# Optimization experiments

Hardware: AMD Instinct MI355X
Metric: run time of the kernel (lower is better)

The kernel has to match this reference:

```python
import jax, jax.numpy as jnp
from jax import lax
import numpy as np

B, S = 128, 512
TARGET_SIZE = 32
T = TARGET_SIZE + 4  # tag_size, START = T-2, END = T-1


def setup_inputs() -> dict:
    key = jax.random.key(0)
    k1, k2, k3, k4 = jax.random.split(key, 4)
    feats = jax.random.normal(k1, (B, S, T), dtype=jnp.float32)
    # contiguous-prefix mask (lengths in [S//2, S])
    lengths = jax.random.randint(k2, (B,), S // 2, S + 1)
    mask = (jnp.arange(S)[None, :] < lengths[:, None]).astype(jnp.int32)
    tags = jax.random.randint(k3, (B, S), 0, TARGET_SIZE).astype(jnp.int32)
    # learned transitions, with the hard constraints from __init__
    transitions = 0.1 * jax.random.normal(k4, (T, T), dtype=jnp.float32)
    transitions = transitions.at[:, T - 2].set(-1000.0)  # nothing -> START
    transitions = transitions.at[T - 1, :].set(-1000.0)  # END -> nothing
    return {"feats": feats, "transitions": transitions, "mask": mask, "tags": tags}


def _nll(feats, transitions, mask, tags):
    # feats: (B,S,T), transitions: (T,T) with [i,j] = score(prev=i -> cur=j)
    b, s, t = feats.shape
    START, END = t - 2, t - 1
    fdtype = feats.dtype

    feats_t = jnp.swapaxes(feats, 0, 1)   # (S,B,T)
    mask_t = jnp.swapaxes(mask, 0, 1)     # (S,B)

    # ---- forward algorithm (partition function) ----
    # scores[t,b,i,j] = feats[b,t,j] + transitions[i,j]
    part0 = feats_t[0] + transitions[START][None, :]  # (B,T): alpha after step 0

    def step(part, xs):
        f_step, m_step = xs  # (B,T), (B,)
        # cur[b,i,j] = feats[b,j] + trans[i,j] + part[b,i]
        cur = f_step[:, None, :] + transitions[None, :, :] + part[:, :, None]
        new_part = jax.nn.logsumexp(cur, axis=1)  # (B,T)
        part = jnp.where(m_step[:, None].astype(bool), new_part, part)
        return part, None

    part, _ = lax.scan(step, part0, (feats_t[1:], mask_t[1:]))
    final = jax.nn.logsumexp(part[:, :, None] + transitions[None, :, :], axis=1)  # (B,T)
    forward_score = jnp.sum(final[:, END])

    # ---- gold score ----
    tags_i = tags.astype(jnp.int32)
    prev_tags = jnp.concatenate(
        [jnp.full((b, 1), START, dtype=jnp.int32), tags_i[:, :-1]], axis=1)  # (B,S)
    emit = jnp.take_along_axis(feats, tags_i[:, :, None], axis=2)[:, :, 0]    # (B,S)
    trans_sc = transitions[prev_tags, tags_i]                                  # (B,S)
    tg_energy = jnp.sum((emit + trans_sc) * mask.astype(fdtype))
    lengths = jnp.sum(mask, axis=1).astype(jnp.int32)                          # (B,)
    end_ids = jnp.take_along_axis(tags_i, (lengths - 1)[:, None], axis=1)[:, 0]
    end_energy = jnp.sum(transitions[end_ids, END])
    gold_score = tg_energy + end_energy

    # average_batch = True
    return (forward_score - gold_score) / jnp.asarray(b, fdtype)


def reference(feats, transitions, mask, tags):
    return _nll(feats, transitions, mask, tags)
```

## Files before the change

kernel.cpp:

```cpp
#include <hip/hip_runtime.h>
#include <hip/hip_bf16.h>


namespace {
constexpr int kB = 128;
constexpr int kS = 512;
constexpr int kT = 36;
constexpr int kStart = 34;
constexpr int kEnd = 35;
constexpr int kP = 16;
constexpr int kL = 32;
constexpr int kHStr = 72;
constexpr int kEStr = 64;

typedef __bf16 bf16x8 __attribute__((ext_vector_type(8)));
typedef __bf16 bf16x4 __attribute__((ext_vector_type(4)));
typedef float f32x4 __attribute__((ext_vector_type(4)));

__device__ __forceinline__ float readlane_f(float v, int lane) {
    return __builtin_bit_cast(float, __builtin_amdgcn_readlane(__builtin_bit_cast(int, v), lane));
}

__device__ __forceinline__ float wave_sum(float v) {
#pragma unroll
    for (int off = 32; off; off >>= 1) v += __shfl_xor(v, off, 64);
    return v;
}

__device__ __forceinline__ int wave_sum_i(int v) {
#pragma unroll
    for (int off = 32; off; off >>= 1) v += __shfl_xor(v, off, 64);
    return v;
}


__global__ __attribute__((amdgpu_flat_work_group_size(64, 64),
                          amdgpu_waves_per_eu(2, 4)))
void crf_chunk_kernel(const float* __restrict__ feats,
                      const float* __restrict__ trans,
                      const int* __restrict__ mask,
                      __bf16* __restrict__ Hws,
                      float* __restrict__ lscws) {
    const int b = blockIdx.x;
    const int p = blockIdx.y;
    const int tid = threadIdx.x;
    const int ln = tid & 15;
    const int quad = tid >> 4;

    __shared__ __align__(16) unsigned short Hlds[48 * kHStr];
    __shared__ __align__(16) float Etab[kL * kEStr];

    const int* mb = mask + b * kS;
    int len = 0;
    for (int k = tid; k < kS; k += 64) len += mb[k];
    len = wave_sum_i(len);

    __bf16* Hout = Hws + (size_t)(b * kP + p) * (kT * kT);
    const int cs = (p == 0) ? 1 : p * kL;
    const int ce = min((p + 1) * kL, len);
    const int nsteps = ce - cs;

    if (nsteps <= 0) {
        for (int idx = tid; idx < kT * kT; idx += 64)
            Hout[idx] = (__bf16)((idx / kT == idx % kT) ? 1.f : 0.f);
        if (tid == 0) lscws[b * kP + p] = 0.f;
        return;
    }

    for (int idx = tid; idx < 48 * kHStr; idx += 64) Hlds[idx] = 0;
    for (int r = tid; r < kT; r += 64) Hlds[r * kHStr + r] = 0x3F80;

    const float* fb = feats + ((size_t)b * kS + cs) * kT;
    for (int tl2 = 0; tl2 < kL; ++tl2)
        Etab[tl2 * kEStr + tid] = (tid < kT) ? __expf(fb[tl2 * kT + tid]) : 1.0f;

    auto afrag = [&](int rt, int kc) {
        bf16x8 r;
        const int j = rt * 16 + ln;
#pragma unroll
        for (int e = 0; e < 8; ++e) {
            const int k = kc * 32 + quad * 8 + e;
            float v = 0.f;
            if (k < kT && j < kT) v = __expf(trans[k * kT + j]);
            r[e] = (__bf16)v;
        }
        return r;
    };
    const bf16x8 a00 = afrag(0, 0), a01 = afrag(0, 1);
    const bf16x8 a10 = afrag(1, 0), a11 = afrag(1, 1);
    const bf16x8 a20 = afrag(2, 0), a21 = afrag(2, 1);

    float logC = 0.f;
    f32x4 c00, c01, c02, c10, c11, c12, c20, c21, c22;
    const f32x4 z = {0.f, 0.f, 0.f, 0.f};

    for (int tl = 0; tl < nsteps; ++tl) {
        const unsigned short sraw = Hlds[kHStr + 1];
#define BRD_LDS(kc, ct) (*(const bf16x8*)&Hlds[((ct)*16 + ln) * kHStr + (kc)*32 + quad * 8])
        const bf16x8 b00 = BRD_LDS(0, 0), b01 = BRD_LDS(0, 1), b02 = BRD_LDS(0, 2);
        const bf16x8 b10 = BRD_LDS(1, 0), b11 = BRD_LDS(1, 1), b12 = BRD_LDS(1, 2);
        const f32x4 e0 = *(const f32x4*)&Etab[tl * kEStr + 0 + quad * 4];
        const f32x4 e1 = *(const f32x4*)&Etab[tl * kEStr + 16 + quad * 4];
        const f32x4 e2 = *(const f32x4*)&Etab[tl * kEStr + 32 + quad * 4];

        c00 = __builtin_amdgcn_mfma_f32_16x16x32_bf16(a00, b00, z, 0, 0, 0);
        c00 = __builtin_amdgcn_mfma_f32_16x16x32_bf16(a01, b10, c00, 0, 0, 0);
        c01 = __builtin_amdgcn_mfma_f32_16x16x32_bf16(a00, b01, z, 0, 0, 0);
        c01 = __builtin_amdgcn_mfma_f32_16x16x32_bf16(a01, b11, c01, 0, 0, 0);
        c02 = __builtin_amdgcn_mfma_f32_16x16x32_bf16(a00, b02, z, 0, 0, 0);
        c02 = __builtin_amdgcn_mfma_f32_16x16x32_bf16(a01, b12, c02, 0, 0, 0);
        c10 = __builtin_amdgcn_mfma_f32_16x16x32_bf16(a10, b00, z, 0, 0, 0);
        c10 = __builtin_amdgcn_mfma_f32_16x16x32_bf16(a11, b10, c10, 0, 0, 0);
        c11 = __builtin_amdgcn_mfma_f32_16x16x32_bf16(a10, b01, z, 0, 0, 0);
        c11 = __builtin_amdgcn_mfma_f32_16x16x32_bf16(a11, b11, c11, 0, 0, 0);
        c12 = __builtin_amdgcn_mfma_f32_16x16x32_bf16(a10, b02, z, 0, 0, 0);
        c12 = __builtin_amdgcn_mfma_f32_16x16x32_bf16(a11, b12, c12, 0, 0, 0);
        c20 = __builtin_amdgcn_mfma_f32_16x16x32_bf16(a20, b00, z, 0, 0, 0);
        c20 = __builtin_amdgcn_mfma_f32_16x16x32_bf16(a21, b10, c20, 0, 0, 0);
        c21 = __builtin_amdgcn_mfma_f32_16x16x32_bf16(a20, b01, z, 0, 0, 0);
        c21 = __builtin_amdgcn_mfma_f32_16x16x32_bf16(a21, b11, c21, 0, 0, 0);
        c22 = __builtin_amdgcn_mfma_f32_16x16x32_bf16(a20, b02, z, 0, 0, 0);
        c22 = __builtin_amdgcn_mfma_f32_16x16x32_bf16(a21, b12, c22, 0, 0, 0);

        float rs = 1.f;
        if ((tl & 3) == 3) {
            const float s = __builtin_bit_cast(float, (unsigned int)sraw << 16);
            rs = __builtin_amdgcn_rcpf(s);
            logC += __logf(s);
        }
        const f32x4 s0 = e0 * rs, s1 = e1 * rs, s2 = e2 * rs;
        c00 *= s0; c01 *= s0; c02 *= s0;
        c10 *= s1; c11 *= s1; c12 *= s1;
        c20 *= s2; c21 *= s2; c22 *= s2;

#define PACKW(cv, rt, ct) {                                                     \
        bf16x4 hw;                                                              \
        hw[0] = (__bf16)cv[0]; hw[1] = (__bf16)cv[1];                           \
        hw[2] = (__bf16)cv[2]; hw[3] = (__bf16)cv[3];                           \
        *(bf16x4*)&Hlds[((ct)*16 + ln) * kHStr + (rt)*16 + quad * 4] = hw; }
        PACKW(c00, 0, 0) PACKW(c01, 0, 1) PACKW(c02, 0, 2)
        PACKW(c10, 1, 0) PACKW(c11, 1, 1) PACKW(c12, 1, 2)
        PACKW(c20, 2, 0) PACKW(c21, 2, 1) PACKW(c22, 2, 2)
    }

#define STORE_T(cv, rt, ct) {                                     \
    const int rr = (ct)*16 + ln;                                  \
    _Pragma("unroll") for (int reg = 0; reg < 4; ++reg) {         \
        const int mm2 = (rt)*16 + quad * 4 + reg;                 \
        if (mm2 < kT && rr < kT) Hout[mm2 * kT + rr] = (__bf16)cv[reg]; } }
    STORE_T(c00, 0, 0) STORE_T(c01, 0, 1) STORE_T(c02, 0, 2)
    STORE_T(c10, 1, 0) STORE_T(c11, 1, 1) STORE_T(c12, 1, 2)
    STORE_T(c20, 2, 0) STORE_T(c21, 2, 1) STORE_T(c22, 2, 2)
    if (tid == 0) lscws[b * kP + p] = logC;
}


#define FORK36(X) \
    X(0,0,0,0) X(1,1,0,1) X(2,2,0,2) X(3,3,0,3) \
    X(4,0,1,0) X(5,1,1,1) X(6,2,1,2) X(7,3,1,3) \
    X(8,0,2,0) X(9,1,2,1) X(10,2,2,2) X(11,3,2,3) \
    X(12,0,3,0) X(13,1,3,1) X(14,2,3,2) X(15,3,3,3) \
    X(16,0,4,0) X(17,1,4,1) X(18,2,4,2) X(19,3,4,3) \
    X(20,0,5,0) X(21,1,5,1) X(22,2,5,2) X(23,3,5,3) \
    X(24,0,6,0) X(25,1,6,1) X(26,2,6,2) X(27,3,6,3) \
    X(28,0,7,0) X(29,1,7,1) X(30,2,7,2) X(31,3,7,3) \
    X(32,0,8,0) X(33,1,8,1) X(34,2,8,2) X(35,3,8,3)

__global__ __attribute__((amdgpu_flat_work_group_size(64, 64),
                          amdgpu_waves_per_eu(1, 1)))
void crf_combine_kernel(const float* __restrict__ feats,
                        const float* __restrict__ trans,
                        const int* __restrict__ mask,
                        const int* __restrict__ tags,
                        const __bf16* __restrict__ Hws,
                        const float* __restrict__ lscws,
                        float* __restrict__ out) {
    const int b = blockIdx.x;
    const int j = threadIdx.x;
    const float* fbase = feats + (size_t)b * kS * kT;
    const int* mb = mask + b * kS;
    const int* tb = tags + b * kS;

    int len = 0;
    for (int k = j; k < kS; k += 64) len += mb[k];
    len = wave_sum_i(len);

    const float ME = (j < kT) ? __expf(trans[j * kT + kEnd]) : 0.f;

    float a0 = -1e30f;
    if (j < kT) a0 = fbase[j] + trans[kStart * kT + j];
    float C = readlane_f(a0, 0);
    float q = __expf(a0 - C);

    const int jr = (j < kT) ? j : 0;
#pragma unroll
    for (int p = 0; p < kP; ++p) {
        const __bf16* rp = Hws + ((size_t)(b * kP + p) * kT + jr) * kT;
        const bf16x4 h0 = *(const bf16x4*)(rp + 0);
        const bf16x4 h1 = *(const bf16x4*)(rp + 4);
        const bf16x4 h2 = *(const bf16x4*)(rp + 8);
        const bf16x4 h3 = *(const bf16x4*)(rp + 12);
        const bf16x4 h4 = *(const bf16x4*)(rp + 16);
        const bf16x4 h5 = *(const bf16x4*)(rp + 20);
        const bf16x4 h6 = *(const bf16x4*)(rp + 24);
        const bf16x4 h7 = *(const bf16x4*)(rp + 28);
        const bf16x4 h8 = *(const bf16x4*)(rp + 32);
#define BRD2(n, a, g, c) const float bb##n = readlane_f(q, n);
        FORK36(BRD2)
#undef BRD2
        float v0 = 0.f, v1 = 0.f, v2 = 0.f, v3 = 0.f;
#define FMA2(n, a, g, c) v##a = fmaf(bb##n, (float)h##g[c], v##a);
        FORK36(FMA2)
#undef FMA2
        const float qn = (v0 + v1) + (v2 + v3);
        q = (j < kT) ? qn : 0.f;
        C += lscws[b * kP + p];
        const float s = readlane_f(q, 0);
        q *= __builtin_amdgcn_rcpf(s);
        C += __logf(s);
    }

    const float ssum = wave_sum(q * ME);
    const float forward_b = C + __logf(ssum);

    float g = 0.f;
    for (int k = j; k < kS; k += 64) {
        if (k < len) {
            const int tg = tb[k];
            const int pv = (k == 0) ? kStart : tb[k - 1];
            g += fbase[(size_t)k * kT + tg] + trans[pv * kT + tg];
        }
    }
    g = wave_sum(g);

    if (j == 0) {
        g += trans[tb[len - 1] * kT + kEnd];
        atomicAdd(out, (forward_b - g) * (1.0f / kB));
    }
}

}

extern "C" void kernel_launch(void* const* d_in, const int* in_sizes, int n_in,
                              void* d_out, int out_size, void* d_ws, size_t ws_size,
                              hipStream_t stream) {
    const float* feats = (const float*)d_in[0];
    const float* trans = (const float*)d_in[1];
    const int* mask = (const int*)d_in[2];
    const int* tags = (const int*)d_in[3];
    float* out = (float*)d_out;

    __bf16* Hws = (__bf16*)d_ws;
    float* lscws = (float*)(Hws + (size_t)kB * kP * kT * kT);

    (void)hipMemsetAsync(out, 0, sizeof(float), stream);
    crf_chunk_kernel<<<dim3(kB, kP), dim3(64), 0, stream>>>(feats, trans, mask, Hws, lscws);
    crf_combine_kernel<<<dim3(kB), dim3(64), 0, stream>>>(feats, trans, mask, tags,
                                                          Hws, lscws, out);
}
```

Baseline: 109.6 us.

## Keep chunk matrix product in registers using 16x16x16 MFMA, dropping LDS round-trip

```diff
diff --git a/kernel.cpp b/kernel.cpp
--- a/kernel.cpp
+++ b/kernel.cpp
@@ -10,11 +10,10 @@
 constexpr int kEnd = 35;
 constexpr int kP = 16;
 constexpr int kL = 32;
-constexpr int kHStr = 72;
-constexpr int kEStr = 64;
-
-typedef __bf16 bf16x8 __attribute__((ext_vector_type(8)));
+constexpr int kEStr = 48;
+
 typedef __bf16 bf16x4 __attribute__((ext_vector_type(4)));
+typedef short short4 __attribute__((ext_vector_type(4)));
 typedef float f32x4 __attribute__((ext_vector_type(4)));
 
 __device__ __forceinline__ float readlane_f(float v, int lane) {
@@ -32,6 +31,8 @@
     for (int off = 32; off; off >>= 1) v += __shfl_xor(v, off, 64);
     return v;
 }
+
+#define MF16(a, b, c) __builtin_amdgcn_mfma_f32_16x16x16bf16_1k((a), (b), (c), 0, 0, 0)
 
 
 __global__ __attribute__((amdgpu_flat_work_group_size(64, 64),
@@ -47,7 +48,6 @@
     const int ln = tid & 15;
     const int quad = tid >> 4;
 
-    __shared__ __align__(16) unsigned short Hlds[48 * kHStr];
     __shared__ __align__(16) float Etab[kL * kEStr];
 
     const int* mb = mask + b * kS;
@@ -67,90 +67,88 @@
         return;
     }
 
-    for (int idx = tid; idx < 48 * kHStr; idx += 64) Hlds[idx] = 0;
-    for (int r = tid; r < kT; r += 64) Hlds[r * kHStr + r] = 0x3F80;
-
     const float* fb = feats + ((size_t)b * kS + cs) * kT;
-    for (int tl2 = 0; tl2 < kL; ++tl2)
-        Etab[tl2 * kEStr + tid] = (tid < kT) ? __expf(fb[tl2 * kT + tid]) : 1.0f;
+    for (int idx = tid; idx < kL * kEStr; idx += 64) {
+        const int tl = idx / kEStr, jj = idx % kEStr;
+        Etab[idx] = (jj < kT) ? __expf(fb[tl * kT + jj]) : 1.0f;
+    }
+    __builtin_amdgcn_s_waitcnt(0);
 
     auto afrag = [&](int rt, int kc) {
-        bf16x8 r;
-        const int j = rt * 16 + ln;
-#pragma unroll
-        for (int e = 0; e < 8; ++e) {
-            const int k = kc * 32 + quad * 8 + e;
+        bf16x4 r;
+        const int m = rt * 16 + ln;
+#pragma unroll
+        for (int e = 0; e < 4; ++e) {
+            const int k = kc * 16 + quad * 4 + e;
             float v = 0.f;
-            if (k < kT && j < kT) v = __expf(trans[k * kT + j]);
+            if (m < kT && k < kT) v = __expf(trans[k * kT + m]);
             r[e] = (__bf16)v;
         }
-        return r;
+        return __builtin_bit_cast(short4, r);
     };
-    const bf16x8 a00 = afrag(0, 0), a01 = afrag(0, 1);
-    const bf16x8 a10 = afrag(1, 0), a11 = afrag(1, 1);
-    const bf16x8 a20 = afrag(2, 0), a21 = afrag(2, 1);
+    const short4 a00 = afrag(0, 0), a01 = afrag(0, 1), a02 = afrag(0, 2);
+    const short4 a10 = afrag(1, 0), a11 = afrag(1, 1), a12 = afrag(1, 2);
+    const short4 a20 = afrag(2, 0), a21 = afrag(2, 1), a22 = afrag(2, 2);
+
+    auto binit = [&](int kc, int ct) {
+        bf16x4 r;
+        const int n = ct * 16 + ln;
+#pragma unroll
+        for (int e = 0; e < 4; ++e) {
+            const int k = kc * 16 + quad * 4 + e;
+            r[e] = (__bf16)((k == n && k < kT) ? 1.f : 0.f);
+        }
+        return __builtin_bit_cast(short4, r);
+    };
+    short4 b00 = binit(0, 0), b01 = binit(0, 1), b02 = binit(0, 2);
+    short4 b10 = binit(1, 0), b11 = binit(1, 1), b12 = binit(1, 2);
+    short4 b20 = binit(2, 0), b21 = binit(2, 1), b22 = binit(2, 2);
 
     float logC = 0.f;
-    f32x4 c00, c01, c02, c10, c11, c12, c20, c21, c22;
     const f32x4 z = {0.f, 0.f, 0.f, 0.f};
-
     for (int tl = 0; tl < nsteps; ++tl) {
-        const unsigned short sraw = Hlds[kHStr + 1];
-#define BRD_LDS(kc, ct) (*(const bf16x8*)&Hlds[((ct)*16 + ln) * kHStr + (kc)*32 + quad * 8])
-        const bf16x8 b00 = BRD_LDS(0, 0), b01 = BRD_LDS(0, 1), b02 = BRD_LDS(0, 2);
-        const bf16x8 b10 = BRD_LDS(1, 0), b11 = BRD_LDS(1, 1), b12 = BRD_LDS(1, 2);
         const f32x4 e0 = *(const f32x4*)&Etab[tl * kEStr + 0 + quad * 4];
         const f32x4 e1 = *(const f32x4*)&Etab[tl * kEStr + 16 + quad * 4];
         const f32x4 e2 = *(const f32x4*)&Etab[tl * kEStr + 32 + quad * 4];
 
-        c00 = __builtin_amdgcn_mfma_f32_16x16x32_bf16(a00, b00, z, 0, 0, 0);
-        c00 = __builtin_amdgcn_mfma_f32_16x16x32_bf16(a01, b10, c00, 0, 0, 0);
-        c01 = __builtin_amdgcn_mfma_f32_16x16x32_bf16(a00, b01, z, 0, 0, 0);
-        c01 = __builtin_amdgcn_mfma_f32_16x16x32_bf16(a01, b11, c01, 0, 0, 0);
-        c02 = __builtin_amdgcn_mfma_f32_16x16x32_bf16(a00, b02, z, 0, 0, 0);
-        c02 = __builtin_amdgcn_mfma_f32_16x16x32_bf16(a01, b12, c02, 0, 0, 0);
-        c10 = __builtin_amdgcn_mfma_f32_16x16x32_bf16(a10, b00, z, 0, 0, 0);
-        c10 = __builtin_amdgcn_mfma_f32_16x16x32_bf16(a11, b10, c10, 0, 0, 0);
-        c11 = __builtin_amdgcn_mfma_f32_16x16x32_bf16(a10, b01, z, 0, 0, 0);
-        c11 = __builtin_amdgcn_mfma_f32_16x16x32_bf16(a11, b11, c11, 0, 0, 0);
-        c12 = __builtin_amdgcn_mfma_f32_16x16x32_bf16(a10, b02, z, 0, 0, 0);
-        c12 = __builtin_amdgcn_mfma_f32_16x16x32_bf16(a11, b12, c12, 0, 0, 0);
-        c20 = __builtin_amdgcn_mfma_f32_16x16x32_bf16(a20, b00, z, 0, 0, 0);
-        c20 = __builtin_amdgcn_mfma_f32_16x16x32_bf16(a21, b10, c20, 0, 0, 0);
-        c21 = __builtin_amdgcn_mfma_f32_16x16x32_bf16(a20, b01, z, 0, 0, 0);
-        c21 = __builtin_amdgcn_mfma_f32_16x16x32_bf16(a21, b11, c21, 0, 0, 0);
-        c22 = __builtin_amdgcn_mfma_f32_16x16x32_bf16(a20, b02, z, 0, 0, 0);
-        c22 = __builtin_amdgcn_mfma_f32_16x16x32_bf16(a21, b12, c22, 0, 0, 0);
+        f32x4 c00 = MF16(a00, b00, z); f32x4 c01 = MF16(a00, b01, z); f32x4 c02 = MF16(a00, b02, z);
+        c00 = MF16(a01, b10, c00);     c01 = MF16(a01, b11, c01);     c02 = MF16(a01, b12, c02);
+        c00 = MF16(a02, b20, c00);     c01 = MF16(a02, b21, c01);     c02 = MF16(a02, b22, c02);
+        f32x4 c10 = MF16(a10, b00, z); f32x4 c11 = MF16(a10, b01, z); f32x4 c12 = MF16(a10, b02, z);
+        c10 = MF16(a11, b10, c10);     c11 = MF16(a11, b11, c11);     c12 = MF16(a11, b12, c12);
+        c10 = MF16(a12, b20, c10);     c11 = MF16(a12, b21, c11);     c12 = MF16(a12, b22, c12);
+        f32x4 c20 = MF16(a20, b00, z); f32x4 c21 = MF16(a20, b01, z); f32x4 c22 = MF16(a20, b02, z);
+        c20 = MF16(a21, b10, c20);     c21 = MF16(a21, b11, c21);     c22 = MF16(a21, b12, c22);
+        c20 = MF16(a22, b20, c20);     c21 = MF16(a22, b21, c21);     c22 = MF16(a22, b22, c22);
 
         float rs = 1.f;
         if ((tl & 3) == 3) {
-            const float s = __builtin_bit_cast(float, (unsigned int)sraw << 16);
+            const float s = readlane_f(c00[1], 1);
             rs = __builtin_amdgcn_rcpf(s);
             logC += __logf(s);
         }
         const f32x4 s0 = e0 * rs, s1 = e1 * rs, s2 = e2 * rs;
-        c00 *= s0; c01 *= s0; c02 *= s0;
-        c10 *= s1; c11 *= s1; c12 *= s1;
-        c20 *= s2; c21 *= s2; c22 *= s2;
-
-#define PACKW(cv, rt, ct) {                                                     \
-        bf16x4 hw;                                                              \
-        hw[0] = (__bf16)cv[0]; hw[1] = (__bf16)cv[1];                           \
-        hw[2] = (__bf16)cv[2]; hw[3] = (__bf16)cv[3];                           \
-        *(bf16x4*)&Hlds[((ct)*16 + ln) * kHStr + (rt)*16 + quad * 4] = hw; }
-        PACKW(c00, 0, 0) PACKW(c01, 0, 1) PACKW(c02, 0, 2)
-        PACKW(c10, 1, 0) PACKW(c11, 1, 1) PACKW(c12, 1, 2)
-        PACKW(c20, 2, 0) PACKW(c21, 2, 1) PACKW(c22, 2, 2)
-    }
-
-#define STORE_T(cv, rt, ct) {                                     \
-    const int rr = (ct)*16 + ln;                                  \
-    _Pragma("unroll") for (int reg = 0; reg < 4; ++reg) {         \
-        const int mm2 = (rt)*16 + quad * 4 + reg;                 \
-        if (mm2 < kT && rr < kT) Hout[mm2 * kT + rr] = (__bf16)cv[reg]; } }
-    STORE_T(c00, 0, 0) STORE_T(c01, 0, 1) STORE_T(c02, 0, 2)
-    STORE_T(c10, 1, 0) STORE_T(c11, 1, 1) STORE_T(c12, 1, 2)
-    STORE_T(c20, 2, 0) STORE_T(c21, 2, 1) STORE_T(c22, 2, 2)
+
+#define PK(cv, sv) ({ const f32x4 t_ = (cv) * (sv); bf16x4 h_;                  \
+        h_[0] = (__bf16)t_[0]; h_[1] = (__bf16)t_[1];                           \
+        h_[2] = (__bf16)t_[2]; h_[3] = (__bf16)t_[3];                           \
+        __builtin_bit_cast(short4, h_); })
+        b00 = PK(c00, s0); b01 = PK(c01, s0); b02 = PK(c02, s0);
+        b10 = PK(c10, s1); b11 = PK(c11, s1); b12 = PK(c12, s1);
+        b20 = PK(c20, s2); b21 = PK(c21, s2); b22 = PK(c22, s2);
+#undef PK
+    }
+
+#define STOREB(Bv, kc, ct) {                                                    \
+    const bf16x4 h_ = __builtin_bit_cast(bf16x4, Bv);                           \
+    const int n_ = (ct)*16 + ln;                                                \
+    _Pragma("unroll") for (int e = 0; e < 4; ++e) {                             \
+        const int m_ = (kc)*16 + quad * 4 + e;                                  \
+        if (m_ < kT && n_ < kT) Hout[m_ * kT + n_] = h_[e]; } }
+    STOREB(b00, 0, 0) STOREB(b01, 0, 1) STOREB(b02, 0, 2)
+    STOREB(b10, 1, 0) STOREB(b11, 1, 1) STOREB(b12, 1, 2)
+    STOREB(b20, 2, 0) STOREB(b21, 2, 1) STOREB(b22, 2, 2)
+#undef STOREB
     if (tid == 0) lscws[b * kP + p] = logC;
 }
 
```

Result: no change. 111.4 us (+1.6%).
